# Kernel tuning notes

Measured on AMD Instinct MI355X. Metric: run time of the kernel, lower is better.

## Reference

```python
import jax, jax.numpy as jnp
import numpy as np

NUM_ITERATIONS = 5
BIG = 1e30


def _compute_cv(vc, Hf, norm):
    # vc: [B, M, N]; Hf: [M, N] float 0/1 mask; norm: scalar normalization factor
    # sign part: product of signs of incoming messages per check, redistributed
    sign_info = (1.0 - Hf)[None] + vc            # non-edges -> +1 so they don't affect the product
    s = jnp.sign(sign_info)
    row_sign = jnp.prod(s, axis=2, keepdims=True)  # [B, M, 1]
    result_sign = row_sign * Hf * s              # extrinsic sign per edge (self sign divided out)
    # magnitude part: min / second-min over edges of each check (masked top-2)
    back = jnp.where(Hf == 0.0, -BIG - 1.0, 0.0)[None]  # push non-edges to -inf-ish
    a = jnp.clip(jnp.abs(vc), 0.0, BIG)
    decision = -a + back                          # top-2 of this = two smallest magnitudes on edges
    top2 = jax.lax.top_k(decision, 2)[0]          # [B, M, 2]
    mn = (-top2[:, :, 0:1]) * Hf                  # smallest magnitude, broadcast on edges
    sub = (-top2[:, :, 1:2]) * Hf                 # second smallest
    res = jnp.where(a > mn, mn, sub)              # extrinsic min (exclude self if self is the min)
    return norm * res * jax.lax.stop_gradient(result_sign)


def setup_inputs() -> dict:
    key = jax.random.key(0)
    k1, k2, k3 = jax.random.split(key, 3)
    B, M, N = 16, 1024, 2048
    soft_input = jax.random.normal(k1, (B, N), dtype=jnp.float32) * 2.0
    # sparse binary parity-check matrix (Tanner graph), ~20 ones per row, min degree 2
    H = (jax.random.uniform(k2, (M, N)) < 0.01).astype(jnp.int32)
    H = H.at[:, :2].set(1)
    labels = jax.random.randint(k3, (B, N), 0, 2).astype(jnp.int32)
    w = jnp.full((1,), -0.048, dtype=jnp.float32)
    return {"soft_input": soft_input, "H": H, "labels": labels, "w": w}


def reference(soft_input, H, labels, w):
    Hf = H.astype(jnp.float32)
    norm = jax.nn.softplus(w)  # NMS-1 normalized factor, shape [1]
    soft_output = soft_input
    for _ in range(NUM_ITERATIONS):
        vc = soft_output[:, None, :] * Hf          # variable-to-check messages [B, M, N]
        cv = _compute_cv(vc, Hf, norm)             # check-to-variable messages [B, M, N]
        soft_output = soft_input + jnp.sum(cv, axis=1)  # marginalize
    return soft_output
```

## Files before the change

### kernel.cpp

```cpp
#include <hip/hip_runtime.h>

#define BB 16
#define MM 1024
#define NN 2048
#define RCAP 64
#define CCAP 48
#define NITER 5

__device__ __forceinline__ float signf(float x) {
    return (x > 0.0f) ? 1.0f : ((x < 0.0f) ? -1.0f : 0.0f);
}

__global__ void build_lists(const int4* __restrict__ H4,
                            int* __restrict__ row_deg, int* __restrict__ col_deg,
                            unsigned short* __restrict__ row_cols,
                            unsigned short* __restrict__ col_rows) {
    int idx = blockIdx.x * blockDim.x + threadIdx.x;
    if (idx >= MM * NN / 4) return;
    int4 h = H4[idx];
    int base = idx << 2;
    int m = base >> 11;
    int c0 = base & (NN - 1);
    int hv[4] = {h.x, h.y, h.z, h.w};
#pragma unroll
    for (int k = 0; k < 4; ++k) {
        if (hv[k]) {
            int c = c0 + k;
            int j = atomicAdd(&row_deg[m], 1);
            if (j < RCAP) row_cols[m * RCAP + j] = (unsigned short)c;
            if (c >= 2) {
                int j2 = atomicAdd(&col_deg[c], 1);
                if (j2 < CCAP) col_rows[c * CCAP + j2] = (unsigned short)m;
            }
        }
    }
}

__global__ __launch_bounds__(256)
void phase_a(const float* __restrict__ src,
             const int* __restrict__ row_deg,
             const unsigned short* __restrict__ row_cols,
             float4* __restrict__ stats,
             float* __restrict__ heavy,
             const float* __restrict__ wptr) {
    __shared__ float s_soft[NN];
    __shared__ float s_red[8];
    const int b = blockIdx.x >> 2;
    const int m = ((blockIdx.x & 3) << 8) + threadIdx.x;
    const float norm = log1pf(expf(wptr[0]));

    const float4* src4 = (const float4*)(src + b * NN);
    float4* s4 = (float4*)s_soft;
    s4[threadIdx.x] = src4[threadIdx.x];
    s4[threadIdx.x + 256] = src4[threadIdx.x + 256];
    __syncthreads();

    const int deg = min(row_deg[m], RCAP);
    const unsigned short* rc = row_cols + m * RCAP;
    float sgn = 1.0f, mn = 1e30f, sub = 1e30f;
    for (int j = 0; j < deg; ++j) {
        float x = s_soft[rc[j]];
        sgn *= signf(x);
        float a = fabsf(x);
        if (a < mn) { sub = mn; mn = a; }
        else if (a < sub) { sub = a; }
    }
    const float ns = norm * sgn;
    stats[b * MM + m] = make_float4(ns, mn, sub, 0.0f);

    float x0 = s_soft[0], x1 = s_soft[1];
    float cv0 = ns * ((fabsf(x0) > mn) ? mn : sub) * signf(x0);
    float cv1 = ns * ((fabsf(x1) > mn) ? mn : sub) * signf(x1);
#pragma unroll
    for (int off = 32; off > 0; off >>= 1) {
        cv0 += __shfl_down(cv0, off);
        cv1 += __shfl_down(cv1, off);
    }
    const int lane = threadIdx.x & 63, wv = threadIdx.x >> 6;
    if (lane == 0) { s_red[wv] = cv0; s_red[4 + wv] = cv1; }
    __syncthreads();
    if (threadIdx.x == 0) {
        atomicAdd(&heavy[b * 2 + 0], s_red[0] + s_red[1] + s_red[2] + s_red[3]);
        atomicAdd(&heavy[b * 2 + 1], s_red[4] + s_red[5] + s_red[6] + s_red[7]);
    }
}

__global__ __launch_bounds__(256)
void phase_b(const float* __restrict__ src,
             const float* __restrict__ soft_in,
             float* __restrict__ dst,
             const float4* __restrict__ stats,
             const int* __restrict__ col_deg,
             const unsigned short* __restrict__ col_rows,
             const float* __restrict__ heavy) {
    __shared__ float4 s_st[MM];
    const int b = blockIdx.x >> 3;
    const int n = ((blockIdx.x & 7) << 8) + threadIdx.x;

    const float4* st = stats + b * MM;
#pragma unroll
    for (int i = 0; i < 4; ++i) s_st[threadIdx.x + 256 * i] = st[threadIdx.x + 256 * i];
    __syncthreads();

    float result;
    if (n >= 2) {
        float x = src[b * NN + n];
        float a = fabsf(x), sx = signf(x), acc = 0.0f;
        int cd = min(col_deg[n], CCAP);
        const unsigned short* cl = col_rows + n * CCAP;
        for (int j = 0; j < cd; ++j) {
            float4 s = s_st[cl[j]];
            acc += s.x * ((a > s.y) ? s.y : s.z) * sx;
        }
        result = soft_in[b * NN + n] + acc;
    } else {
        result = soft_in[b * NN + n] + heavy[b * 2 + n];
    }
    dst[b * NN + n] = result;
}

extern "C" void kernel_launch(void* const* d_in, const int* in_sizes, int n_in,
                              void* d_out, int out_size, void* d_ws, size_t ws_size,
                              hipStream_t stream) {
    const float* soft_in = (const float*)d_in[0];
    const int*   H       = (const int*)d_in[1];
    const float* w       = (const float*)d_in[3];
    float* out = (float*)d_out;

    char* ws = (char*)d_ws;
    int*   row_deg  = (int*)ws;
    int*   col_deg  = (int*)(ws + 4096);
    float* heavy    = (float*)(ws + 12288);
    unsigned short* row_cols = (unsigned short*)(ws + 13312);
    unsigned short* col_rows = (unsigned short*)(ws + 13312 + 131072);
    float4* stats   = (float4*)(ws + 13312 + 131072 + 196608);
    float*  soft_buf = (float*)(ws + 13312 + 131072 + 196608 + 262144);

    hipMemsetAsync(ws, 0, 13312, stream);
    build_lists<<<(MM * NN / 4 + 255) / 256, 256, 0, stream>>>(
        (const int4*)H, row_deg, col_deg, row_cols, col_rows);

    const float* src = soft_in;
    for (int it = 0; it < NITER; ++it) {
        float* hv = heavy + it * BB * 2;
        phase_a<<<64, 256, 0, stream>>>(src, row_deg, row_cols, stats, hv, w);
        float* dst = (it == NITER - 1) ? out : soft_buf;
        phase_b<<<128, 256, 0, stream>>>(src, soft_in, dst, stats, col_deg, col_rows, hv);
        src = dst;
    }
}
```

Measured before the change: 144.9 us.

## Fuse all decode phases into one persistent kernel with grid barriers

Replaces the list-building kernel and the ten per-iteration phase kernels with a single persistent kernel of 128 blocks. Phases are separated by atomic-counter grid barriers instead of separate launches. This removes repeated launch overhead and inter-kernel gaps. The trade-offs are that H-list construction now runs on only 128 blocks in a grid-stride loop, and the spin barriers rely on all blocks being co-resident. Phase A also leaves half the blocks idle at each barrier.

```diff
diff --git a/kernel.cpp b/kernel.cpp
--- a/kernel.cpp
+++ b/kernel.cpp
@@ -6,117 +6,136 @@
 #define RCAP 64
 #define CCAP 48
 #define NITER 5
+#define NBLK 128
+#define NTHR 256
 
 __device__ __forceinline__ float signf(float x) {
     return (x > 0.0f) ? 1.0f : ((x < 0.0f) ? -1.0f : 0.0f);
 }
 
-__global__ void build_lists(const int4* __restrict__ H4,
-                            int* __restrict__ row_deg, int* __restrict__ col_deg,
-                            unsigned short* __restrict__ row_cols,
-                            unsigned short* __restrict__ col_rows) {
-    int idx = blockIdx.x * blockDim.x + threadIdx.x;
-    if (idx >= MM * NN / 4) return;
-    int4 h = H4[idx];
-    int base = idx << 2;
-    int m = base >> 11;
-    int c0 = base & (NN - 1);
-    int hv[4] = {h.x, h.y, h.z, h.w};
+__device__ __forceinline__ void grid_barrier(int* cnt, int target) {
+    __threadfence();
+    __syncthreads();
+    if (threadIdx.x == 0) {
+        __hip_atomic_fetch_add(cnt, 1, __ATOMIC_RELEASE, __HIP_MEMORY_SCOPE_AGENT);
+        while (__hip_atomic_load(cnt, __ATOMIC_RELAXED, __HIP_MEMORY_SCOPE_AGENT) < target)
+            __builtin_amdgcn_s_sleep(2);
+        (void)__hip_atomic_load(cnt, __ATOMIC_ACQUIRE, __HIP_MEMORY_SCOPE_AGENT);
+    }
+    __syncthreads();
+}
+
+__global__ __launch_bounds__(NTHR)
+void decode_all(const float* __restrict__ soft_in,
+                const int4* __restrict__ H4,
+                const float* __restrict__ wptr,
+                float* __restrict__ out,
+                int* __restrict__ cnt,
+                int* __restrict__ row_deg, int* __restrict__ col_deg,
+                float* __restrict__ heavy,
+                unsigned short* __restrict__ row_cols,
+                unsigned short* __restrict__ col_rows,
+                float4* __restrict__ stats,
+                float* __restrict__ soft_buf) {
+    __shared__ float4 s_st[MM];
+    __shared__ float s_red[8];
+    float* s_soft = (float*)s_st;
+
+    const int blk = blockIdx.x, t = threadIdx.x;
+    const int lane = t & 63, wv = t >> 6;
+    const float norm = log1pf(expf(wptr[0]));
+
+    for (int idx = blk * NTHR + t; idx < MM * NN / 4; idx += NBLK * NTHR) {
+        int4 h = H4[idx];
+        int base = idx << 2;
+        int m = base >> 11, c0 = base & (NN - 1);
+        int hv[4] = {h.x, h.y, h.z, h.w};
 #pragma unroll
-    for (int k = 0; k < 4; ++k) {
-        if (hv[k]) {
-            int c = c0 + k;
-            int j = atomicAdd(&row_deg[m], 1);
-            if (j < RCAP) row_cols[m * RCAP + j] = (unsigned short)c;
-            if (c >= 2) {
-                int j2 = atomicAdd(&col_deg[c], 1);
-                if (j2 < CCAP) col_rows[c * CCAP + j2] = (unsigned short)m;
+        for (int k = 0; k < 4; ++k) {
+            if (hv[k]) {
+                int c = c0 + k;
+                int j = atomicAdd(&row_deg[m], 1);
+                if (j < RCAP) row_cols[m * RCAP + j] = (unsigned short)c;
+                if (c >= 2) {
+                    int j2 = atomicAdd(&col_deg[c], 1);
+                    if (j2 < CCAP) col_rows[c * CCAP + j2] = (unsigned short)m;
+                }
             }
         }
     }
-}
+    int bar = 0;
+    grid_barrier(cnt, ++bar * NBLK);
 
-__global__ __launch_bounds__(256)
-void phase_a(const float* __restrict__ src,
-             const int* __restrict__ row_deg,
-             const unsigned short* __restrict__ row_cols,
-             float4* __restrict__ stats,
-             float* __restrict__ heavy,
-             const float* __restrict__ wptr) {
-    __shared__ float s_soft[NN];
-    __shared__ float s_red[8];
-    const int b = blockIdx.x >> 2;
-    const int m = ((blockIdx.x & 3) << 8) + threadIdx.x;
-    const float norm = log1pf(expf(wptr[0]));
+    const int ba = blk >> 2;
+    const int m = ((blk & 3) << 8) + t;
+    const int rdeg = (blk < 64) ? min(row_deg[m], RCAP) : 0;
+    const unsigned short* rc = row_cols + m * RCAP;
+    const int bb = blk >> 3;
+    const int n = ((blk & 7) << 8) + t;
+    const int cd = (n >= 2) ? min(col_deg[n], CCAP) : 0;
+    const unsigned short* cl = col_rows + n * CCAP;
 
-    const float4* src4 = (const float4*)(src + b * NN);
-    float4* s4 = (float4*)s_soft;
-    s4[threadIdx.x] = src4[threadIdx.x];
-    s4[threadIdx.x + 256] = src4[threadIdx.x + 256];
-    __syncthreads();
+    const float* src = soft_in;
+    for (int it = 0; it < NITER; ++it) {
+        if (blk < 64) {
+            const float4* src4 = (const float4*)(src + ba * NN);
+            float4* s4 = (float4*)s_soft;
+            s4[t] = src4[t];
+            s4[t + 256] = src4[t + 256];
+            __syncthreads();
 
-    const int deg = min(row_deg[m], RCAP);
-    const unsigned short* rc = row_cols + m * RCAP;
-    float sgn = 1.0f, mn = 1e30f, sub = 1e30f;
-    for (int j = 0; j < deg; ++j) {
-        float x = s_soft[rc[j]];
-        sgn *= signf(x);
-        float a = fabsf(x);
-        if (a < mn) { sub = mn; mn = a; }
-        else if (a < sub) { sub = a; }
+            float sgn = 1.0f, mn = 1e30f, sub = 1e30f;
+            for (int j = 0; j < rdeg; ++j) {
+                float x = s_soft[rc[j]];
+                sgn *= signf(x);
+                float a = fabsf(x);
+                if (a < mn) { sub = mn; mn = a; }
+                else if (a < sub) { sub = a; }
+            }
+            const float ns = norm * sgn;
+            stats[ba * MM + m] = make_float4(ns, mn, sub, 0.0f);
+
+            float x0 = s_soft[0], x1 = s_soft[1];
+            float cv0 = ns * ((fabsf(x0) > mn) ? mn : sub) * signf(x0);
+            float cv1 = ns * ((fabsf(x1) > mn) ? mn : sub) * signf(x1);
+#pragma unroll
+            for (int off = 32; off > 0; off >>= 1) {
+                cv0 += __shfl_down(cv0, off);
+                cv1 += __shfl_down(cv1, off);
+            }
+            if (lane == 0) { s_red[wv] = cv0; s_red[4 + wv] = cv1; }
+            __syncthreads();
+            if (t == 0) {
+                float* hv = heavy + (it * BB + ba) * 2;
+                atomicAdd(&hv[0], s_red[0] + s_red[1] + s_red[2] + s_red[3]);
+                atomicAdd(&hv[1], s_red[4] + s_red[5] + s_red[6] + s_red[7]);
+            }
+        }
+        grid_barrier(cnt, ++bar * NBLK);
+
+        const float4* stb = stats + bb * MM;
+#pragma unroll
+        for (int i = 0; i < 4; ++i) s_st[t + 256 * i] = stb[t + 256 * i];
+        __syncthreads();
+
+        float* dst = (it == NITER - 1) ? out : soft_buf;
+        float result;
+        if (n >= 2) {
+            float x = src[bb * NN + n];
+            float a = fabsf(x), sx = signf(x), acc = 0.0f;
+            for (int j = 0; j < cd; ++j) {
+                float4 s = s_st[cl[j]];
+                acc += s.x * ((a > s.y) ? s.y : s.z) * sx;
+            }
+            result = soft_in[bb * NN + n] + acc;
+        } else {
+            result = soft_in[bb * NN + n] + heavy[(it * BB + bb) * 2 + n];
+        }
+        dst[bb * NN + n] = result;
+
+        src = soft_buf;
+        if (it < NITER - 1) grid_barrier(cnt, ++bar * NBLK);
     }
-    const float ns = norm * sgn;
-    stats[b * MM + m] = make_float4(ns, mn, sub, 0.0f);
-
-    float x0 = s_soft[0], x1 = s_soft[1];
-    float cv0 = ns * ((fabsf(x0) > mn) ? mn : sub) * signf(x0);
-    float cv1 = ns * ((fabsf(x1) > mn) ? mn : sub) * signf(x1);
-#pragma unroll
-    for (int off = 32; off > 0; off >>= 1) {
-        cv0 += __shfl_down(cv0, off);
-        cv1 += __shfl_down(cv1, off);
-    }
-    const int lane = threadIdx.x & 63, wv = threadIdx.x >> 6;
-    if (lane == 0) { s_red[wv] = cv0; s_red[4 + wv] = cv1; }
-    __syncthreads();
-    if (threadIdx.x == 0) {
-        atomicAdd(&heavy[b * 2 + 0], s_red[0] + s_red[1] + s_red[2] + s_red[3]);
-        atomicAdd(&heavy[b * 2 + 1], s_red[4] + s_red[5] + s_red[6] + s_red[7]);
-    }
-}
-
-__global__ __launch_bounds__(256)
-void phase_b(const float* __restrict__ src,
-             const float* __restrict__ soft_in,
-             float* __restrict__ dst,
-             const float4* __restrict__ stats,
-             const int* __restrict__ col_deg,
-             const unsigned short* __restrict__ col_rows,
-             const float* __restrict__ heavy) {
-    __shared__ float4 s_st[MM];
-    const int b = blockIdx.x >> 3;
-    const int n = ((blockIdx.x & 7) << 8) + threadIdx.x;
-
-    const float4* st = stats + b * MM;
-#pragma unroll
-    for (int i = 0; i < 4; ++i) s_st[threadIdx.x + 256 * i] = st[threadIdx.x + 256 * i];
-    __syncthreads();
-
-    float result;
-    if (n >= 2) {
-        float x = src[b * NN + n];
-        float a = fabsf(x), sx = signf(x), acc = 0.0f;
-        int cd = min(col_deg[n], CCAP);
-        const unsigned short* cl = col_rows + n * CCAP;
-        for (int j = 0; j < cd; ++j) {
-            float4 s = s_st[cl[j]];
-            acc += s.x * ((a > s.y) ? s.y : s.z) * sx;
-        }
-        result = soft_in[b * NN + n] + acc;
-    } else {
-        result = soft_in[b * NN + n] + heavy[b * 2 + n];
-    }
-    dst[b * NN + n] = result;
 }
 
 extern "C" void kernel_launch(void* const* d_in, const int* in_sizes, int n_in,
@@ -125,27 +144,19 @@
     const float* soft_in = (const float*)d_in[0];
     const int*   H       = (const int*)d_in[1];
     const float* w       = (const float*)d_in[3];
-    float* out = (float*)d_out;
 
     char* ws = (char*)d_ws;
-    int*   row_deg  = (int*)ws;
-    int*   col_deg  = (int*)(ws + 4096);
-    float* heavy    = (float*)(ws + 12288);
-    unsigned short* row_cols = (unsigned short*)(ws + 13312);
-    unsigned short* col_rows = (unsigned short*)(ws + 13312 + 131072);
-    float4* stats   = (float4*)(ws + 13312 + 131072 + 196608);
-    float*  soft_buf = (float*)(ws + 13312 + 131072 + 196608 + 262144);
+    int*   cnt      = (int*)ws;
+    int*   row_deg  = (int*)(ws + 64);
+    int*   col_deg  = (int*)(ws + 64 + 4096);
+    float* heavy    = (float*)(ws + 64 + 4096 + 8192);
+    unsigned short* row_cols = (unsigned short*)(ws + 13056);
+    unsigned short* col_rows = (unsigned short*)(ws + 13056 + 131072);
+    float4* stats   = (float4*)(ws + 13056 + 131072 + 196608);
+    float*  soft_buf = (float*)(ws + 13056 + 131072 + 196608 + 262144);
 
-    hipMemsetAsync(ws, 0, 13312, stream);
-    build_lists<<<(MM * NN / 4 + 255) / 256, 256, 0, stream>>>(
-        (const int4*)H, row_deg, col_deg, row_cols, col_rows);
-
-    const float* src = soft_in;
-    for (int it = 0; it < NITER; ++it) {
-        float* hv = heavy + it * BB * 2;
-        phase_a<<<64, 256, 0, stream>>>(src, row_deg, row_cols, stats, hv, w);
-        float* dst = (it == NITER - 1) ? out : soft_buf;
-        phase_b<<<128, 256, 0, stream>>>(src, soft_in, dst, stats, col_deg, col_rows, hv);
-        src = dst;
-    }
+    hipMemsetAsync(ws, 0, 13056, stream);
+    decode_all<<<NBLK, NTHR, 0, stream>>>(soft_in, (const int4*)H, w,
+                                          (float*)d_out, cnt, row_deg, col_deg,
+                                          heavy, row_cols, col_rows, stats, soft_buf);
 }
```

Result: slower. 303.4 us (+109.4%).

## Fuse column-accumulate and row-stat phases into per-iteration kernels with redundant recompute

Applied to the files above, without the earlier changes.

Replaces the ten alternating phase_a/phase_b launches with one stats kernel, three fused iteration kernels and one final kernel, cutting the launch count from ten to five plus the build. Each fused block recomputes the full column update for its batch row redundantly, so every chunk has the whole new soft vector locally before computing its share of row statistics. The heavy-column atomics and their accumulator buffer are replaced by in-block reductions. Index lists are read as int4 vectors with masked unrolled loops. The trade is about 4x to 8x duplicated column work per batch and fewer blocks in flight, in exchange for fewer launches and kernel boundaries.

```diff
diff --git a/kernel.cpp b/kernel.cpp
--- a/kernel.cpp
+++ b/kernel.cpp
@@ -5,7 +5,9 @@
 #define NN 2048
 #define RCAP 64
 #define CCAP 48
-#define NITER 5
+#define INFF __builtin_inff()
+
+typedef unsigned short u16;
 
 __device__ __forceinline__ float signf(float x) {
     return (x > 0.0f) ? 1.0f : ((x < 0.0f) ? -1.0f : 0.0f);
@@ -13,110 +15,246 @@
 
 __global__ void build_lists(const int4* __restrict__ H4,
                             int* __restrict__ row_deg, int* __restrict__ col_deg,
-                            unsigned short* __restrict__ row_cols,
-                            unsigned short* __restrict__ col_rows) {
+                            u16* __restrict__ row_cols, u16* __restrict__ col_rows) {
     int idx = blockIdx.x * blockDim.x + threadIdx.x;
     if (idx >= MM * NN / 4) return;
     int4 h = H4[idx];
     int base = idx << 2;
-    int m = base >> 11;
-    int c0 = base & (NN - 1);
+    int m = base >> 11, c0 = base & (NN - 1);
     int hv[4] = {h.x, h.y, h.z, h.w};
 #pragma unroll
     for (int k = 0; k < 4; ++k) {
         if (hv[k]) {
             int c = c0 + k;
             int j = atomicAdd(&row_deg[m], 1);
-            if (j < RCAP) row_cols[m * RCAP + j] = (unsigned short)c;
+            if (j < RCAP) row_cols[m * RCAP + j] = (u16)c;
             if (c >= 2) {
                 int j2 = atomicAdd(&col_deg[c], 1);
-                if (j2 < CCAP) col_rows[c * CCAP + j2] = (unsigned short)m;
+                if (j2 < CCAP) col_rows[c * CCAP + j2] = (u16)m;
             }
         }
     }
 }
 
+__device__ __forceinline__ float4 row_stat(const float* s_soft, const u16* rc,
+                                           int deg, float norm) {
+    float sgn = 1.0f, mn = INFF, sub = INFF;
+    for (int jb = 0; jb < deg; jb += 8) {
+        int4 iv = *(const int4*)(rc + jb);
+        const u16* ip = (const u16*)&iv;
+#pragma unroll
+        for (int k = 0; k < 8; ++k) {
+            float x = s_soft[ip[k] & (NN - 1)];
+            x = (jb + k < deg) ? x : INFF;
+            sgn *= signf(x);
+            float a = fabsf(x);
+            if (a < mn) { sub = mn; mn = a; }
+            else if (a < sub) sub = a;
+        }
+    }
+    return make_float4(norm * sgn, mn, sub, 0.0f);
+}
+
+__device__ __forceinline__ float col_acc(const float4* s_st, const u16* cl,
+                                         int deg, float x) {
+    float a = fabsf(x), sx = signf(x), acc = 0.0f;
+    for (int jb = 0; jb < deg; jb += 8) {
+        int4 iv = *(const int4*)(cl + jb);
+        const u16* ip = (const u16*)&iv;
+#pragma unroll
+        for (int k = 0; k < 8; ++k) {
+            float4 s = s_st[ip[k] & (MM - 1)];
+            float cv = s.x * ((a > s.y) ? s.y : s.z) * sx;
+            acc += (jb + k < deg) ? cv : 0.0f;
+        }
+    }
+    return acc;
+}
+
+__device__ __forceinline__ void block_reduce2(float c0, float c1, float* s_red,
+                                              int t, float& r0, float& r1) {
+    __syncthreads();
+#pragma unroll
+    for (int off = 32; off; off >>= 1) { c0 += __shfl_down(c0, off); c1 += __shfl_down(c1, off); }
+    int lane = t & 63, wv = t >> 6;
+    if (lane == 0) { s_red[wv] = c0; s_red[4 + wv] = c1; }
+    __syncthreads();
+    r0 = s_red[0] + s_red[1] + s_red[2] + s_red[3];
+    r1 = s_red[4] + s_red[5] + s_red[6] + s_red[7];
+}
+
 __global__ __launch_bounds__(256)
-void phase_a(const float* __restrict__ src,
-             const int* __restrict__ row_deg,
-             const unsigned short* __restrict__ row_cols,
-             float4* __restrict__ stats,
-             float* __restrict__ heavy,
-             const float* __restrict__ wptr) {
+void stats_first(const float* __restrict__ soft_in,
+                 const int* __restrict__ row_deg, const u16* __restrict__ row_cols,
+                 float4* __restrict__ stats_out, const float* __restrict__ wptr) {
     __shared__ float s_soft[NN];
+    const int b = blockIdx.x >> 2, t = threadIdx.x;
+    const int m = ((blockIdx.x & 3) << 8) + t;
+    const float norm = log1pf(expf(wptr[0]));
+    const float4* sp = (const float4*)(soft_in + b * NN);
+    float4* d = (float4*)s_soft;
+    d[t] = sp[t]; d[t + 256] = sp[t + 256];
+    __syncthreads();
+    stats_out[b * MM + m] = row_stat(s_soft, row_cols + m * RCAP,
+                                     min(row_deg[m], RCAP), norm);
+}
+
+__global__ __launch_bounds__(256)
+void iter_fused(const float* __restrict__ soft_in,
+                const float* __restrict__ soft_old,
+                const float4* __restrict__ stats_prev,
+                float4* __restrict__ stats_new,
+                float* __restrict__ soft_cur_out,
+                const int* __restrict__ row_deg, const u16* __restrict__ row_cols,
+                const int* __restrict__ col_deg, const u16* __restrict__ col_rows,
+                const float* __restrict__ wptr) {
+    __shared__ float4 s_st[MM];
+    __shared__ float s_old[NN];
+    __shared__ float s_new[NN];
     __shared__ float s_red[8];
-    const int b = blockIdx.x >> 2;
-    const int m = ((blockIdx.x & 3) << 8) + threadIdx.x;
+    const int b = blockIdx.x >> 2, t = threadIdx.x, chunk = blockIdx.x & 3;
     const float norm = log1pf(expf(wptr[0]));
 
-    const float4* src4 = (const float4*)(src + b * NN);
-    float4* s4 = (float4*)s_soft;
-    s4[threadIdx.x] = src4[threadIdx.x];
-    s4[threadIdx.x + 256] = src4[threadIdx.x + 256];
-    __syncthreads();
-
-    const int deg = min(row_deg[m], RCAP);
-    const unsigned short* rc = row_cols + m * RCAP;
-    float sgn = 1.0f, mn = 1e30f, sub = 1e30f;
-    for (int j = 0; j < deg; ++j) {
-        float x = s_soft[rc[j]];
-        sgn *= signf(x);
-        float a = fabsf(x);
-        if (a < mn) { sub = mn; mn = a; }
-        else if (a < sub) { sub = a; }
-    }
-    const float ns = norm * sgn;
-    stats[b * MM + m] = make_float4(ns, mn, sub, 0.0f);
-
-    float x0 = s_soft[0], x1 = s_soft[1];
-    float cv0 = ns * ((fabsf(x0) > mn) ? mn : sub) * signf(x0);
-    float cv1 = ns * ((fabsf(x1) > mn) ? mn : sub) * signf(x1);
-#pragma unroll
-    for (int off = 32; off > 0; off >>= 1) {
-        cv0 += __shfl_down(cv0, off);
-        cv1 += __shfl_down(cv1, off);
-    }
-    const int lane = threadIdx.x & 63, wv = threadIdx.x >> 6;
-    if (lane == 0) { s_red[wv] = cv0; s_red[4 + wv] = cv1; }
-    __syncthreads();
-    if (threadIdx.x == 0) {
-        atomicAdd(&heavy[b * 2 + 0], s_red[0] + s_red[1] + s_red[2] + s_red[3]);
-        atomicAdd(&heavy[b * 2 + 1], s_red[4] + s_red[5] + s_red[6] + s_red[7]);
-    }
+    {
+        const float4* sp = stats_prev + b * MM;
+#pragma unroll
+        for (int i = 0; i < 4; ++i) s_st[t + 256 * i] = sp[t + 256 * i];
+        const float4* so = (const float4*)(soft_old + b * NN);
+        float4* d = (float4*)s_old;
+        d[t] = so[t]; d[t + 256] = so[t + 256];
+    }
+    __syncthreads();
+
+    float c0 = 0.0f, c1 = 0.0f;
+    {
+        float x0 = s_old[0], x1 = s_old[1];
+        float a0 = fabsf(x0), sx0 = signf(x0), a1 = fabsf(x1), sx1 = signf(x1);
+#pragma unroll
+        for (int i = 0; i < 4; ++i) {
+            float4 s = s_st[t + 256 * i];
+            c0 += s.x * ((a0 > s.y) ? s.y : s.z) * sx0;
+            c1 += s.x * ((a1 > s.y) ? s.y : s.z) * sx1;
+        }
+    }
+    float r0, r1;
+    block_reduce2(c0, c1, s_red, t, r0, r1);
+
+    float vals[8];
+#pragma unroll
+    for (int i = 0; i < 8; ++i) {
+        int n = t + 256 * i;
+        if (n >= 2) {
+            vals[i] = soft_in[b * NN + n] +
+                      col_acc(s_st, col_rows + n * CCAP, min(col_deg[n], CCAP), s_old[n]);
+        } else {
+            vals[i] = soft_in[b * NN + n] + ((n == 0) ? r0 : r1);
+        }
+    }
+    __syncthreads();
+#pragma unroll
+    for (int i = 0; i < 8; ++i) s_new[t + 256 * i] = vals[i];
+    __syncthreads();
+
+    if (chunk == 0) {
+        const float4* sn = (const float4*)s_new;
+        float4* o = (float4*)(soft_cur_out + b * NN);
+        o[t] = sn[t]; o[t + 256] = sn[t + 256];
+    }
+
+    const int m = (chunk << 8) + t;
+    stats_new[b * MM + m] = row_stat(s_new, row_cols + m * RCAP,
+                                     min(row_deg[m], RCAP), norm);
 }
 
 __global__ __launch_bounds__(256)
-void phase_b(const float* __restrict__ src,
-             const float* __restrict__ soft_in,
-             float* __restrict__ dst,
-             const float4* __restrict__ stats,
-             const int* __restrict__ col_deg,
-             const unsigned short* __restrict__ col_rows,
-             const float* __restrict__ heavy) {
+void final_fused(const float* __restrict__ soft_in,
+                 const float* __restrict__ soft_old,
+                 const float4* __restrict__ stats_prev,
+                 float* __restrict__ out,
+                 const int* __restrict__ row_deg, const u16* __restrict__ row_cols,
+                 const int* __restrict__ col_deg, const u16* __restrict__ col_rows,
+                 const float* __restrict__ wptr) {
     __shared__ float4 s_st[MM];
-    const int b = blockIdx.x >> 3;
-    const int n = ((blockIdx.x & 7) << 8) + threadIdx.x;
-
-    const float4* st = stats + b * MM;
-#pragma unroll
-    for (int i = 0; i < 4; ++i) s_st[threadIdx.x + 256 * i] = st[threadIdx.x + 256 * i];
-    __syncthreads();
-
-    float result;
+    __shared__ float s_old[NN];
+    __shared__ float s_new[NN];
+    __shared__ float s_red[8];
+    const int b = blockIdx.x >> 3, t = threadIdx.x, chunk = blockIdx.x & 7;
+    const float norm = log1pf(expf(wptr[0]));
+
+    {
+        const float4* sp = stats_prev + b * MM;
+#pragma unroll
+        for (int i = 0; i < 4; ++i) s_st[t + 256 * i] = sp[t + 256 * i];
+        const float4* so = (const float4*)(soft_old + b * NN);
+        float4* d = (float4*)s_old;
+        d[t] = so[t]; d[t + 256] = so[t + 256];
+    }
+    __syncthreads();
+
+    float c0 = 0.0f, c1 = 0.0f;
+    {
+        float x0 = s_old[0], x1 = s_old[1];
+        float a0 = fabsf(x0), sx0 = signf(x0), a1 = fabsf(x1), sx1 = signf(x1);
+#pragma unroll
+        for (int i = 0; i < 4; ++i) {
+            float4 s = s_st[t + 256 * i];
+            c0 += s.x * ((a0 > s.y) ? s.y : s.z) * sx0;
+            c1 += s.x * ((a1 > s.y) ? s.y : s.z) * sx1;
+        }
+    }
+    float r0, r1;
+    block_reduce2(c0, c1, s_red, t, r0, r1);
+
+    float vals[8];
+#pragma unroll
+    for (int i = 0; i < 8; ++i) {
+        int n = t + 256 * i;
+        if (n >= 2) {
+            vals[i] = soft_in[b * NN + n] +
+                      col_acc(s_st, col_rows + n * CCAP, min(col_deg[n], CCAP), s_old[n]);
+        } else {
+            vals[i] = soft_in[b * NN + n] + ((n == 0) ? r0 : r1);
+        }
+    }
+    __syncthreads();
+#pragma unroll
+    for (int i = 0; i < 8; ++i) s_new[t + 256 * i] = vals[i];
+    __syncthreads();
+
+    float4 st5[4];
+#pragma unroll
+    for (int i = 0; i < 4; ++i) {
+        int m = t + 256 * i;
+        st5[i] = row_stat(s_new, row_cols + m * RCAP, min(row_deg[m], RCAP), norm);
+    }
+    __syncthreads();
+#pragma unroll
+    for (int i = 0; i < 4; ++i) s_st[t + 256 * i] = st5[i];
+    __syncthreads();
+
+    float h0 = 0.0f, h1 = 0.0f;
+    {
+        float x0 = s_new[0], x1 = s_new[1];
+        float a0 = fabsf(x0), sx0 = signf(x0), a1 = fabsf(x1), sx1 = signf(x1);
+#pragma unroll
+        for (int i = 0; i < 4; ++i) {
+            float4 s = s_st[t + 256 * i];
+            h0 += s.x * ((a0 > s.y) ? s.y : s.z) * sx0;
+            h1 += s.x * ((a1 > s.y) ? s.y : s.z) * sx1;
+        }
+    }
+    float q0, q1;
+    block_reduce2(h0, h1, s_red, t, q0, q1);
+
+    const int n = (chunk << 8) + t;
+    float res;
     if (n >= 2) {
-        float x = src[b * NN + n];
-        float a = fabsf(x), sx = signf(x), acc = 0.0f;
-        int cd = min(col_deg[n], CCAP);
-        const unsigned short* cl = col_rows + n * CCAP;
-        for (int j = 0; j < cd; ++j) {
-            float4 s = s_st[cl[j]];
-            acc += s.x * ((a > s.y) ? s.y : s.z) * sx;
-        }
-        result = soft_in[b * NN + n] + acc;
+        res = soft_in[b * NN + n] +
+              col_acc(s_st, col_rows + n * CCAP, min(col_deg[n], CCAP), s_new[n]);
     } else {
-        result = soft_in[b * NN + n] + heavy[b * 2 + n];
-    }
-    dst[b * NN + n] = result;
+        res = soft_in[b * NN + n] + ((n == 0) ? q0 : q1);
+    }
+    out[b * NN + n] = res;
 }
 
 extern "C" void kernel_launch(void* const* d_in, const int* in_sizes, int n_in,
@@ -128,24 +266,26 @@
     float* out = (float*)d_out;
 
     char* ws = (char*)d_ws;
-    int*   row_deg  = (int*)ws;
-    int*   col_deg  = (int*)(ws + 4096);
-    float* heavy    = (float*)(ws + 12288);
-    unsigned short* row_cols = (unsigned short*)(ws + 13312);
-    unsigned short* col_rows = (unsigned short*)(ws + 13312 + 131072);
-    float4* stats   = (float4*)(ws + 13312 + 131072 + 196608);
-    float*  soft_buf = (float*)(ws + 13312 + 131072 + 196608 + 262144);
-
-    hipMemsetAsync(ws, 0, 13312, stream);
+    int* row_deg = (int*)ws;
+    int* col_deg = (int*)(ws + 4096);
+    u16* row_cols = (u16*)(ws + 12288);
+    u16* col_rows = (u16*)(ws + 143360);
+    float4* statsA = (float4*)(ws + 339968);
+    float4* statsB = (float4*)(ws + 602112);
+    float* softX = (float*)(ws + 864256);
+    float* softY = (float*)(ws + 995328);
+
+    hipMemsetAsync(ws, 0, 12288, stream);
     build_lists<<<(MM * NN / 4 + 255) / 256, 256, 0, stream>>>(
         (const int4*)H, row_deg, col_deg, row_cols, col_rows);
 
-    const float* src = soft_in;
-    for (int it = 0; it < NITER; ++it) {
-        float* hv = heavy + it * BB * 2;
-        phase_a<<<64, 256, 0, stream>>>(src, row_deg, row_cols, stats, hv, w);
-        float* dst = (it == NITER - 1) ? out : soft_buf;
-        phase_b<<<128, 256, 0, stream>>>(src, soft_in, dst, stats, col_deg, col_rows, hv);
-        src = dst;
-    }
-}
+    stats_first<<<64, 256, 0, stream>>>(soft_in, row_deg, row_cols, statsA, w);
+    iter_fused<<<64, 256, 0, stream>>>(soft_in, soft_in, statsA, statsB, softX,
+                                       row_deg, row_cols, col_deg, col_rows, w);
+    iter_fused<<<64, 256, 0, stream>>>(soft_in, softX, statsB, statsA, softY,
+                                       row_deg, row_cols, col_deg, col_rows, w);
+    iter_fused<<<64, 256, 0, stream>>>(soft_in, softY, statsA, statsB, softX,
+                                       row_deg, row_cols, col_deg, col_rows, w);
+    final_fused<<<128, 256, 0, stream>>>(soft_in, softX, statsB, out,
+                                         row_deg, row_cols, col_deg, col_rows, w);
+}
```

After: 164.0 us. 1.13x slower.
